# Kernel optimization log

Measured on AMD Instinct MI355X. Metric: run time of the kernel, lower is better.

The kernel has to match this reference:

```python
import jax, jax.numpy as jnp
import numpy as np

B = 524288
IN_DIM = 16
OUT_DIM = 32  # hidden_dim3
N_CHUNKS = 4
CHUNK = 4


def ste_round(x):
    # straight-through round (grad passes unchanged, like Round.apply)
    return x + jax.lax.stop_gradient(jnp.round(x) - x)


def ste_sign(x):
    # straight-through sign (grad passes unchanged, like Sign.apply)
    return x + jax.lax.stop_gradient(jnp.sign(x) - x)


def setup_inputs() -> dict:
    key = jax.random.key(0)
    k1, k2 = jax.random.split(key)
    Input = jax.random.uniform(k1, (B, IN_DIM), dtype=jnp.float32)
    weight = jax.random.normal(k2, (OUT_DIM, IN_DIM), dtype=jnp.float32)
    InMin = jnp.float32(0.0)
    InMax = jnp.float32(1.0)
    return {"Input": Input, "weight": weight, "InMin": InMin, "InMax": InMax}


def reference(Input, weight, InMin, InMax):
    # eval-mode forward of QuantLinear
    scale = InMax - InMin
    w = ste_sign(weight)                       # [O, I] in {-1, 0, 1}
    wP = jax.nn.relu(w)                        # positive mask
    wM = jax.nn.relu(-w)                       # negative mask

    # 4-bit input quantization (eval path): clip(round((x-min)/(max-min)*15), 0, 15)
    q = jnp.clip(ste_round((Input - InMin) / scale * 15.0), 0.0, 15.0)  # [B, I]

    # bias = linear(InMin * ones, w): each row = InMin * sum_j w[o, j]
    bias = InMin * jnp.sum(w, axis=1)          # [O], broadcasts over batch

    # chunked 4-wide linears, vectorized over the 4 chunks
    qc = q.reshape(B, N_CHUNKS, CHUNK)         # [B, C, 4]
    wPc = wP.reshape(OUT_DIM, N_CHUNKS, CHUNK)  # [O, C, 4]
    wMc = wM.reshape(OUT_DIM, N_CHUNKS, CHUNK)
    yP = jnp.einsum('bcf,ocf->cbo', qc, wPc)   # [C, B, O]
    yM = jnp.einsum('bcf,ocf->cbo', qc, wMc)   # [C, B, O]

    # accumulate clip(round(y/15), -4, 4) * (InMax - InMin) over all 8 terms
    terms = jnp.clip(ste_round(yP / 15.0), -4.0, 4.0) \
          + jnp.clip(ste_round(-yM / 15.0), -4.0, 4.0)  # [C, B, O]
    x = jnp.sum(terms, axis=0) * scale + bias  # [B, O]
    return x
```

## Files before the change

kernel.cpp:

```cpp
#include <hip/hip_runtime.h>
#include <stdint.h>


#if __has_builtin(__builtin_amdgcn_sdot4)
#define HAVE_SDOT4 1
#else
#define HAVE_SDOT4 0
#endif

__device__ __forceinline__ int dot7(uint32_t q, uint32_t m) {
#if HAVE_SDOT4
    return __builtin_amdgcn_sdot4((int)q, (int)m, 7, false);
#else
    return (int)(((q & m) * 0x01010101u) >> 24) + 7;
#endif
}

__device__ __forceinline__ int r15(int y7) {
    return (int)(((uint32_t)y7 * 274u) >> 12);
}

__global__ __launch_bounds__(256, 6) void qlin_kernel(
    const float* __restrict__ in, const float* __restrict__ wgt,
    const float* __restrict__ pmin, const float* __restrict__ pmax,
    float* __restrict__ out, int nrows)
{
    __shared__ uint4 smask[64];
    __shared__ __align__(16) float sbias[32];

    const int t = threadIdx.x;
    const float InMin = pmin[0];
    const float InMax = pmax[0];
    const float scale = __fsub_rn(InMax, InMin);

    const uint32_t MASKBYTE = HAVE_SDOT4 ? 1u : 0xFFu;

    {
        int o = t >> 3, k = t & 7, c = k & 3, isM = k >> 2;
        const float* wrow = wgt + o * 16 + c * 4;
        uint32_t m = 0;
#pragma unroll
        for (int j = 0; j < 4; ++j) {
            float v = wrow[j];
            bool sel = isM ? (v < 0.0f) : (v > 0.0f);
            if (sel) m |= MASKBYTE << (8 * j);
        }
        ((uint32_t*)smask)[o * 8 + isM * 4 + c] = m;
    }
    __syncthreads();
    if (t < 32) {
        const uint32_t* mo = (const uint32_t*)smask + t * 8;
        int s = 0;
#pragma unroll
        for (int c = 0; c < 4; ++c)
            s += __popc(mo[c]) - __popc(mo[4 + c]);
        if (!HAVE_SDOT4) s /= 8;
        sbias[t] = __fmul_rn(InMin, (float)s);
    }
    __syncthreads();

    const int lane = t & 63;
    const int ogrp = lane & 7;
    const int rsel = lane >> 3;
    const int srcb = rsel << 2;

    const uint4 MP0 = smask[(ogrp * 4 + 0) * 2], MM0 = smask[(ogrp * 4 + 0) * 2 + 1];
    const uint4 MP1 = smask[(ogrp * 4 + 1) * 2], MM1 = smask[(ogrp * 4 + 1) * 2 + 1];
    const uint4 MP2 = smask[(ogrp * 4 + 2) * 2], MM2 = smask[(ogrp * 4 + 2) * 2 + 1];
    const uint4 MP3 = smask[(ogrp * 4 + 3) * 2], MM3 = smask[(ogrp * 4 + 3) * 2 + 1];
    const float4 bias = *(const float4*)(sbias + ogrp * 4);

    const bool unit = (scale == 1.0f);
    const int gw = blockIdx.x * (256 >> 6) + (t >> 6);
    const int nw = gridDim.x * (256 >> 6);

    for (int R = gw * 16; R < nrows; R += nw * 16) {
        const float4 f = *((const float4*)in + (size_t)R * 4 + lane);

        float e[4] = { f.x, f.y, f.z, f.w };
        uint32_t qw = 0;
#pragma unroll
        for (int j = 0; j < 4; ++j) {
            float d  = __fsub_rn(e[j], InMin);
            float sd = unit ? d : __fdiv_rn(d, scale);
            float v  = __fmul_rn(sd, 15.0f);
            float rr = rintf(v);
            rr = fminf(fmaxf(rr, 0.0f), 15.0f);
            qw |= ((uint32_t)(int)rr) << (8 * j);
        }

        const uint32_t qA0 = __shfl(qw, srcb + 0, 64);
        const uint32_t qA1 = __shfl(qw, srcb + 1, 64);
        const uint32_t qA2 = __shfl(qw, srcb + 2, 64);
        const uint32_t qA3 = __shfl(qw, srcb + 3, 64);
        const uint32_t qB0 = __shfl(qw, 32 + srcb + 0, 64);
        const uint32_t qB1 = __shfl(qw, 32 + srcb + 1, 64);
        const uint32_t qB2 = __shfl(qw, 32 + srcb + 2, 64);
        const uint32_t qB3 = __shfl(qw, 32 + srcb + 3, 64);

        float* p0 = out + (size_t)(R + rsel) * 32 + (ogrp << 2);

#define ROWCOMP(q0, q1, q2, q3, dst)                                        \
        {                                                                   \
            int a0 = r15(dot7(q0, MP0.x)) - r15(dot7(q0, MM0.x))            \
                   + r15(dot7(q1, MP0.y)) - r15(dot7(q1, MM0.y))            \
                   + r15(dot7(q2, MP0.z)) - r15(dot7(q2, MM0.z))            \
                   + r15(dot7(q3, MP0.w)) - r15(dot7(q3, MM0.w));           \
            int a1 = r15(dot7(q0, MP1.x)) - r15(dot7(q0, MM1.x))            \
                   + r15(dot7(q1, MP1.y)) - r15(dot7(q1, MM1.y))            \
                   + r15(dot7(q2, MP1.z)) - r15(dot7(q2, MM1.z))            \
                   + r15(dot7(q3, MP1.w)) - r15(dot7(q3, MM1.w));           \
            int a2 = r15(dot7(q0, MP2.x)) - r15(dot7(q0, MM2.x))            \
                   + r15(dot7(q1, MP2.y)) - r15(dot7(q1, MM2.y))            \
                   + r15(dot7(q2, MP2.z)) - r15(dot7(q2, MM2.z))            \
                   + r15(dot7(q3, MP2.w)) - r15(dot7(q3, MM2.w));           \
            int a3 = r15(dot7(q0, MP3.x)) - r15(dot7(q0, MM3.x))            \
                   + r15(dot7(q1, MP3.y)) - r15(dot7(q1, MM3.y))            \
                   + r15(dot7(q2, MP3.z)) - r15(dot7(q2, MM3.z))            \
                   + r15(dot7(q3, MP3.w)) - r15(dot7(q3, MM3.w));           \
            float4 res;                                                     \
            res.x = __fadd_rn(__fmul_rn((float)a0, scale), bias.x);         \
            res.y = __fadd_rn(__fmul_rn((float)a1, scale), bias.y);         \
            res.z = __fadd_rn(__fmul_rn((float)a2, scale), bias.z);         \
            res.w = __fadd_rn(__fmul_rn((float)a3, scale), bias.w);         \
            *(float4*)(dst) = res;                                          \
        }

        ROWCOMP(qA0, qA1, qA2, qA3, p0);
        ROWCOMP(qB0, qB1, qB2, qB3, p0 + 8 * 32);
#undef ROWCOMP
    }
}

extern "C" void kernel_launch(void* const* d_in, const int* in_sizes, int n_in,
                              void* d_out, int out_size, void* d_ws, size_t ws_size,
                              hipStream_t stream) {
    (void)n_in; (void)d_ws; (void)ws_size; (void)out_size;
    const float* in  = (const float*)d_in[0];
    const float* wgt = (const float*)d_in[1];
    const float* mn  = (const float*)d_in[2];
    const float* mx  = (const float*)d_in[3];
    float* out = (float*)d_out;
    const int nrows = in_sizes[0] / 16;
    const int blocks = 2048;
    qlin_kernel<<<blocks, 256, 0, stream>>>(in, wgt, mn, mx, out, nrows);
}
```

Baseline: 107.5 us.

## Issue all input loads before mask setup, one-shot 64 rows per wave

```diff
diff --git a/kernel.cpp b/kernel.cpp
--- a/kernel.cpp
+++ b/kernel.cpp
@@ -20,7 +20,7 @@
     return (int)(((uint32_t)y7 * 274u) >> 12);
 }
 
-__global__ __launch_bounds__(256, 6) void qlin_kernel(
+__global__ __launch_bounds__(256) void qlin_kernel(
     const float* __restrict__ in, const float* __restrict__ wgt,
     const float* __restrict__ pmin, const float* __restrict__ pmax,
     float* __restrict__ out, int nrows)
@@ -29,6 +29,20 @@
     __shared__ __align__(16) float sbias[32];
 
     const int t = threadIdx.x;
+    const int lane = t & 63;
+    const int wave = (blockIdx.x << 2) + (t >> 6);
+    const size_t R0 = (size_t)wave * 64;
+
+    const float4* inp = (const float4*)in + R0 * 4 + lane;
+    float4 f0, f1, f2, f3;
+    const bool live = (long)R0 < (long)nrows;
+    if (live) {
+        f0 = inp[0];
+        f1 = inp[64];
+        f2 = inp[128];
+        f3 = inp[192];
+    }
+
     const float InMin = pmin[0];
     const float InMax = pmax[0];
     const float scale = __fsub_rn(InMax, InMin);
@@ -59,7 +73,8 @@
     }
     __syncthreads();
 
-    const int lane = t & 63;
+    if (!live) return;
+
     const int ogrp = lane & 7;
     const int rsel = lane >> 3;
     const int srcb = rsel << 2;
@@ -71,34 +86,22 @@
     const float4 bias = *(const float4*)(sbias + ogrp * 4);
 
     const bool unit = (scale == 1.0f);
-    const int gw = blockIdx.x * (256 >> 6) + (t >> 6);
-    const int nw = gridDim.x * (256 >> 6);
 
-    for (int R = gw * 16; R < nrows; R += nw * 16) {
-        const float4 f = *((const float4*)in + (size_t)R * 4 + lane);
-
-        float e[4] = { f.x, f.y, f.z, f.w };
-        uint32_t qw = 0;
-#pragma unroll
-        for (int j = 0; j < 4; ++j) {
-            float d  = __fsub_rn(e[j], InMin);
-            float sd = unit ? d : __fdiv_rn(d, scale);
-            float v  = __fmul_rn(sd, 15.0f);
-            float rr = rintf(v);
-            rr = fminf(fmaxf(rr, 0.0f), 15.0f);
-            qw |= ((uint32_t)(int)rr) << (8 * j);
-        }
-
-        const uint32_t qA0 = __shfl(qw, srcb + 0, 64);
-        const uint32_t qA1 = __shfl(qw, srcb + 1, 64);
-        const uint32_t qA2 = __shfl(qw, srcb + 2, 64);
-        const uint32_t qA3 = __shfl(qw, srcb + 3, 64);
-        const uint32_t qB0 = __shfl(qw, 32 + srcb + 0, 64);
-        const uint32_t qB1 = __shfl(qw, 32 + srcb + 1, 64);
-        const uint32_t qB2 = __shfl(qw, 32 + srcb + 2, 64);
-        const uint32_t qB3 = __shfl(qw, 32 + srcb + 3, 64);
-
-        float* p0 = out + (size_t)(R + rsel) * 32 + (ogrp << 2);
+#define QUANT(F, QW)                                                        \
+    {                                                                       \
+        float e[4] = { F.x, F.y, F.z, F.w };                                \
+        uint32_t pk = 0;                                                    \
+        _Pragma("unroll")                                                   \
+        for (int j = 0; j < 4; ++j) {                                       \
+            float d  = __fsub_rn(e[j], InMin);                              \
+            float sd = unit ? d : __fdiv_rn(d, scale);                      \
+            float v  = __fmul_rn(sd, 15.0f);                                \
+            float rr = rintf(v);                                            \
+            rr = fminf(fmaxf(rr, 0.0f), 15.0f);                             \
+            pk |= ((uint32_t)(int)rr) << (8 * j);                           \
+        }                                                                   \
+        QW = pk;                                                            \
+    }
 
 #define ROWCOMP(q0, q1, q2, q3, dst)                                        \
         {                                                                   \
@@ -126,10 +129,31 @@
             *(float4*)(dst) = res;                                          \
         }
 
-        ROWCOMP(qA0, qA1, qA2, qA3, p0);
-        ROWCOMP(qB0, qB1, qB2, qB3, p0 + 8 * 32);
+#define SLAB(F, K)                                                          \
+    {                                                                       \
+        uint32_t qw;                                                        \
+        QUANT(F, qw);                                                       \
+        const uint32_t qA0 = __shfl(qw, srcb + 0, 64);                      \
+        const uint32_t qA1 = __shfl(qw, srcb + 1, 64);                      \
+        const uint32_t qA2 = __shfl(qw, srcb + 2, 64);                      \
+        const uint32_t qA3 = __shfl(qw, srcb + 3, 64);                      \
+        const uint32_t qB0 = __shfl(qw, 32 + srcb + 0, 64);                 \
+        const uint32_t qB1 = __shfl(qw, 32 + srcb + 1, 64);                 \
+        const uint32_t qB2 = __shfl(qw, 32 + srcb + 2, 64);                 \
+        const uint32_t qB3 = __shfl(qw, 32 + srcb + 3, 64);                 \
+        float* p0 = out + (R0 + (size_t)(K)*16 + rsel) * 32 + (ogrp << 2);  \
+        ROWCOMP(qA0, qA1, qA2, qA3, p0);                                    \
+        ROWCOMP(qB0, qB1, qB2, qB3, p0 + 8 * 32);                           \
+    }
+
+    SLAB(f0, 0)
+    SLAB(f1, 1)
+    SLAB(f2, 2)
+    SLAB(f3, 3)
+
+#undef SLAB
 #undef ROWCOMP
-    }
+#undef QUANT
 }
 
 extern "C" void kernel_launch(void* const* d_in, const int* in_sizes, int n_in,
@@ -142,6 +166,6 @@
     const float* mx  = (const float*)d_in[3];
     float* out = (float*)d_out;
     const int nrows = in_sizes[0] / 16;
-    const int blocks = 2048;
+    const int blocks = (nrows + 255) / 256;
     qlin_kernel<<<blocks, 256, 0, stream>>>(in, wgt, mn, mx, out, nrows);
 }
```

Result: no change. 106.3 us (-1.1%).
